# Optimization experiments

Hardware: AMD Instinct MI355X
Metric: run time of the kernel (lower is better)

Reference implementation:

```python
import jax, jax.numpy as jnp
import numpy as np

NUM_USERS = 100000
NUM_ITEMS = 200000
D = 128          # embedding_dim
K = 4            # num interest heads
B = 4096
H = 256          # history length
H1, H2 = 512, 256  # hidden_units


def setup_inputs() -> dict:
    key = jax.random.key(0)
    ks = jax.random.split(key, 10)
    inp = {
        "user_ids": jax.random.randint(ks[0], (B,), 0, NUM_USERS),
        "candidate_items": jax.random.randint(ks[1], (B,), 0, NUM_ITEMS),
        "history_items": jax.random.randint(ks[2], (B, H), 0, NUM_ITEMS),
        "item_table": jax.random.normal(ks[3], (NUM_ITEMS, D), dtype=jnp.float32) * 0.05,
        "Wp": jax.random.normal(ks[4], (D, K), dtype=jnp.float32) * (1.0 / np.sqrt(D)),
        "W1": jax.random.normal(ks[5], (2 * D, H1), dtype=jnp.float32) * (1.0 / np.sqrt(2 * D)),
        "b1": jnp.zeros((H1,), dtype=jnp.float32),
        "W2": jax.random.normal(ks[6], (H1, H2), dtype=jnp.float32) * (1.0 / np.sqrt(H1)),
        "b2": jnp.zeros((H2,), dtype=jnp.float32),
        "W3": jax.random.normal(ks[7], (H2, 1), dtype=jnp.float32) * (1.0 / np.sqrt(H2)),
        "b3": jnp.zeros((1,), dtype=jnp.float32),
    }
    return inp


def reference(user_ids, candidate_items, history_items, item_table, Wp,
              W1, b1, W2, b2, W3, b3):
    # user_ids is unused by the original forward (user_emb never applied)
    item_vecs = item_table[history_items]          # (B, H, D)
    cand_vec = item_table[candidate_items]         # (B, D)

    # per-interest attention scores, softmax over history axis
    scores = jnp.einsum('bhd,dk->bhk', item_vecs, Wp)   # (B, H, K)
    scores = jax.nn.softmax(scores, axis=1)

    # softmax-weighted pooling -> K interest vectors per user
    interest_vectors = jnp.einsum('bhk,bhd->bkd', scores, item_vecs)  # (B, K, D)

    # similarity to candidate, pick best interest (data-dependent gather)
    sim_scores = jnp.einsum('bkd,bd->bk', interest_vectors, cand_vec)  # (B, K)
    best_idx = jnp.argmax(sim_scores, axis=-1)                          # (B,)
    selected = jnp.take_along_axis(
        interest_vectors, best_idx[:, None, None], axis=1)[:, 0, :]    # (B, D)

    # MLP tail: [2D -> 512] ReLU [512 -> 256] ReLU [256 -> 1], sigmoid
    x = jnp.concatenate([selected, cand_vec], axis=-1)  # (B, 2D)
    x = jax.nn.relu(x @ W1 + b1)
    x = jax.nn.relu(x @ W2 + b2)
    out = (x @ W3 + b3)[:, 0]                            # (B,)
    return jax.nn.sigmoid(out)
```

## Files before the change

### kernel.cpp

```cpp
#include <hip/hip_runtime.h>
#include <hip/hip_bf16.h>
#include <math.h>

#define B_SZ   4096
#define H_LEN  256
#define D_DIM  128
#define K_HEADS 4
#define H1_DIM 512
#define H2_DIM 256

#define CH     64
#define NCH    4
#define TPAD   132

typedef __attribute__((ext_vector_type(8))) short bf16x8;
typedef __attribute__((ext_vector_type(4))) float f32x4;

__global__ __launch_bounds__(256, 4) void interest_kernel(
    const int*   __restrict__ cand_ids,
    const int*   __restrict__ hist,
    const float* __restrict__ table,
    const float* __restrict__ Wp,
    __hip_bfloat16* __restrict__ Xbf)
{
    __shared__ float tile[CH * TPAD];
    __shared__ float wpt[K_HEADS * D_DIM];
    __shared__ float exps4[CH * 4];
    __shared__ float candv[D_DIM];
    __shared__ int   rowids[H_LEN];
    __shared__ float lsumW[16];
    __shared__ float simred[4][K_HEADS];
    __shared__ int   bestk;

    const int b    = blockIdx.x;
    const int t    = threadIdx.x;
    const int lane = t & 63, w = t >> 6;
    const int r    = t >> 2, q = t & 3;
    const int d    = t & 127, half = t >> 7;

    if (t < D_DIM) {
        float4 w4 = ((const float4*)Wp)[t];
        wpt[0 * D_DIM + t] = w4.x;
        wpt[1 * D_DIM + t] = w4.y;
        wpt[2 * D_DIM + t] = w4.z;
        wpt[3 * D_DIM + t] = w4.w;
    }
    const int cand = cand_ids[b];
    if (t >= 128 && t < 160) {
        int c = t - 128;
        ((float4*)candv)[c] = ((const float4*)(table + (long long)cand * D_DIM))[c];
    }
    rowids[t] = hist[(long long)b * H_LEN + t];

    __syncthreads();

    float a0 = 0.f, a1 = 0.f, a2 = 0.f, a3 = 0.f;
    float l0 = 0.f, l1 = 0.f, l2 = 0.f, l3 = 0.f;

    float4 v0, v1, v2, v3, v4, v5, v6, v7;
    {
        const int row = rowids[r];
        const float* rp = table + (long long)row * D_DIM + (q << 2);
        v0 = *(const float4*)(rp + 0 * 16);
        v1 = *(const float4*)(rp + 1 * 16);
        v2 = *(const float4*)(rp + 2 * 16);
        v3 = *(const float4*)(rp + 3 * 16);
        v4 = *(const float4*)(rp + 4 * 16);
        v5 = *(const float4*)(rp + 5 * 16);
        v6 = *(const float4*)(rp + 6 * 16);
        v7 = *(const float4*)(rp + 7 * 16);
    }

    #pragma unroll
    for (int c = 0; c < NCH; ++c) {
        float4 u0, u1, u2, u3, u4, u5, u6, u7;
        if (c + 1 < NCH) {
            const int row = rowids[((c + 1) << 6) + r];
            const float* rp = table + (long long)row * D_DIM + (q << 2);
            u0 = *(const float4*)(rp + 0 * 16);
            u1 = *(const float4*)(rp + 1 * 16);
            u2 = *(const float4*)(rp + 2 * 16);
            u3 = *(const float4*)(rp + 3 * 16);
            u4 = *(const float4*)(rp + 4 * 16);
            u5 = *(const float4*)(rp + 5 * 16);
            u6 = *(const float4*)(rp + 6 * 16);
            u7 = *(const float4*)(rp + 7 * 16);
        }

        float s0 = 0.f, s1 = 0.f, s2 = 0.f, s3 = 0.f;
        float4 va;
        #define DO_J(J, VV)                                                     \
        {   va = VV;                                                            \
            const int cb = (q << 2) + (J << 4);                                 \
            float4 w0 = *(const float4*)(wpt + 0 * D_DIM + cb);                 \
            float4 w1 = *(const float4*)(wpt + 1 * D_DIM + cb);                 \
            float4 w2 = *(const float4*)(wpt + 2 * D_DIM + cb);                 \
            float4 w3 = *(const float4*)(wpt + 3 * D_DIM + cb);                 \
            s0 += va.x * w0.x + va.y * w0.y + va.z * w0.z + va.w * w0.w;        \
            s1 += va.x * w1.x + va.y * w1.y + va.z * w1.z + va.w * w1.w;        \
            s2 += va.x * w2.x + va.y * w2.y + va.z * w2.z + va.w * w2.w;        \
            s3 += va.x * w3.x + va.y * w3.y + va.z * w3.z + va.w * w3.w;        \
            *(float4*)(tile + (t >> 2) * TPAD + cb) = va;                       \
        }
        DO_J(0, v0) DO_J(1, v1) DO_J(2, v2) DO_J(3, v3)
        DO_J(4, v4) DO_J(5, v5) DO_J(6, v6) DO_J(7, v7)
        #undef DO_J

        s0 += __shfl_xor(s0, 1); s0 += __shfl_xor(s0, 2);
        s1 += __shfl_xor(s1, 1); s1 += __shfl_xor(s1, 2);
        s2 += __shfl_xor(s2, 1); s2 += __shfl_xor(s2, 2);
        s3 += __shfl_xor(s3, 1); s3 += __shfl_xor(s3, 2);

        float e0 = expf(s0), e1 = expf(s1), e2 = expf(s2), e3 = expf(s3);
        if (q == 0) ((float4*)exps4)[r] = make_float4(e0, e1, e2, e3);

        float t0 = e0, t1 = e1, t2 = e2, t3 = e3;
        #pragma unroll
        for (int off = 4; off <= 32; off <<= 1) {
            t0 += __shfl_xor(t0, off);
            t1 += __shfl_xor(t1, off);
            t2 += __shfl_xor(t2, off);
            t3 += __shfl_xor(t3, off);
        }
        l0 += t0; l1 += t1; l2 += t2; l3 += t3;

        __syncthreads();

        #pragma unroll 8
        for (int i = 0; i < 32; ++i) {
            int hl = (half << 5) + i;
            float4 e4 = ((const float4*)exps4)[hl];
            float  vv = tile[hl * TPAD + d];
            a0 += e4.x * vv; a1 += e4.y * vv; a2 += e4.z * vv; a3 += e4.w * vv;
        }

        __syncthreads();

        v0 = u0; v1 = u1; v2 = u2; v3 = u3;
        v4 = u4; v5 = u5; v6 = u6; v7 = u7;
    }

    float* partBp = tile;
    float* ivbufp = tile + 512;

    if (half == 1) ((float4*)partBp)[d] = make_float4(a0, a1, a2, a3);
    if (lane == 0) ((float4*)lsumW)[w]  = make_float4(l0, l1, l2, l3);
    __syncthreads();

    float s0 = 0.f, s1 = 0.f, s2 = 0.f, s3 = 0.f;
    if (half == 0) {
        float4 pb = ((const float4*)partBp)[d];
        float4 L0 = ((const float4*)lsumW)[0];
        float4 L1 = ((const float4*)lsumW)[1];
        float4 L2 = ((const float4*)lsumW)[2];
        float4 L3 = ((const float4*)lsumW)[3];
        float i0 = 1.f / (L0.x + L1.x + L2.x + L3.x);
        float i1 = 1.f / (L0.y + L1.y + L2.y + L3.y);
        float i2 = 1.f / (L0.z + L1.z + L2.z + L3.z);
        float i3 = 1.f / (L0.w + L1.w + L2.w + L3.w);
        a0 = (a0 + pb.x) * i0;
        a1 = (a1 + pb.y) * i1;
        a2 = (a2 + pb.z) * i2;
        a3 = (a3 + pb.w) * i3;
        ((float4*)ivbufp)[d] = make_float4(a0, a1, a2, a3);
        float cd = candv[d];
        s0 = a0 * cd; s1 = a1 * cd; s2 = a2 * cd; s3 = a3 * cd;
    }
    #pragma unroll
    for (int off = 32; off >= 1; off >>= 1) {
        s0 += __shfl_xor(s0, off);
        s1 += __shfl_xor(s1, off);
        s2 += __shfl_xor(s2, off);
        s3 += __shfl_xor(s3, off);
    }
    if (lane == 0) {
        simred[w][0] = s0; simred[w][1] = s1;
        simred[w][2] = s2; simred[w][3] = s3;
    }
    __syncthreads();

    if (t == 0) {
        float sim[4];
        #pragma unroll
        for (int k = 0; k < 4; ++k)
            sim[k] = simred[0][k] + simred[1][k] + simred[2][k] + simred[3][k];
        int best = 0;
        #pragma unroll
        for (int k = 1; k < 4; ++k) if (sim[k] > sim[best]) best = k;
        bestk = best;
    }
    __syncthreads();

    __hip_bfloat16* xrow = Xbf + (long long)b * (2 * D_DIM);
    if (t < 128) xrow[t] = __float2bfloat16(ivbufp[t * 4 + bestk]);
    else         xrow[t] = __float2bfloat16(candv[t - 128]);
}

__global__ __launch_bounds__(256) void convert_weights(
    const float* __restrict__ W1, const float* __restrict__ W2,
    __hip_bfloat16* __restrict__ W1t, __hip_bfloat16* __restrict__ W2t)
{
    __shared__ float tl[32][33];
    int bid = blockIdx.x;
    const float* W; __hip_bfloat16* Wt; int K, N;
    if (bid < 128) { W = W1; Wt = W1t; K = 2 * D_DIM; N = H1_DIM; }
    else           { W = W2; Wt = W2t; K = H1_DIM;    N = H2_DIM; bid -= 128; }
    const int ntn = N >> 5;
    const int k0 = (bid / ntn) << 5, n0 = (bid % ntn) << 5;
    const int tx = threadIdx.x & 31, ty = threadIdx.x >> 5;
    #pragma unroll
    for (int j = 0; j < 4; ++j)
        tl[ty + 8 * j][tx] = W[(long long)(k0 + ty + 8 * j) * N + n0 + tx];
    __syncthreads();
    #pragma unroll
    for (int j = 0; j < 4; ++j)
        Wt[(long long)(n0 + ty + 8 * j) * K + k0 + tx] =
            __float2bfloat16(tl[tx][ty + 8 * j]);
}

__global__ __launch_bounds__(512) void mlp_fused(
    const __hip_bfloat16* __restrict__ X,
    const __hip_bfloat16* __restrict__ W1t,
    const float* __restrict__ b1,
    const __hip_bfloat16* __restrict__ W2t,
    const float* __restrict__ b2,
    const float* __restrict__ W3,
    const float* __restrict__ b3,
    float*       __restrict__ out)
{
    __shared__ __hip_bfloat16 h1[16][H1_DIM + 8];
    __shared__ float          h2[16][H2_DIM + 4];

    const int t    = threadIdx.x;
    const int wave = t >> 6, lane = t & 63;
    const int lm   = lane & 15, quad = lane >> 4;
    const int m0   = blockIdx.x * 16;

    const __hip_bfloat16* Ap = X + (long long)(m0 + lm) * (2 * D_DIM) + quad * 8;
    bf16x8 af[8];
    #pragma unroll
    for (int it = 0; it < 8; ++it) af[it] = *(const bf16x8*)(Ap + it * 32);

    #pragma unroll
    for (int tn = 0; tn < 4; ++tn) {
        const int n0 = (wave * 4 + tn) * 16;
        const __hip_bfloat16* Bp = W1t + (long long)(n0 + lm) * (2 * D_DIM) + quad * 8;
        f32x4 acc = {0.f, 0.f, 0.f, 0.f};
        #pragma unroll
        for (int it = 0; it < 8; ++it) {
            bf16x8 bfr = *(const bf16x8*)(Bp + it * 32);
            acc = __builtin_amdgcn_mfma_f32_16x16x32_bf16(af[it], bfr, acc, 0, 0, 0);
        }
        const float bv = b1[n0 + lm];
        #pragma unroll
        for (int i = 0; i < 4; ++i)
            h1[quad * 4 + i][n0 + lm] = __float2bfloat16(fmaxf(acc[i] + bv, 0.f));
    }
    __syncthreads();

    bf16x8 a2[16];
    #pragma unroll
    for (int it = 0; it < 16; ++it)
        a2[it] = *(const bf16x8*)(&h1[lm][quad * 8 + it * 32]);

    #pragma unroll
    for (int tn = 0; tn < 2; ++tn) {
        const int n0 = (wave * 2 + tn) * 16;
        const __hip_bfloat16* Bp = W2t + (long long)(n0 + lm) * H1_DIM + quad * 8;
        f32x4 acc = {0.f, 0.f, 0.f, 0.f};
        #pragma unroll
        for (int it = 0; it < 16; ++it) {
            bf16x8 bfr = *(const bf16x8*)(Bp + it * 32);
            acc = __builtin_amdgcn_mfma_f32_16x16x32_bf16(a2[it], bfr, acc, 0, 0, 0);
        }
        const float bv = b2[n0 + lm];
        #pragma unroll
        for (int i = 0; i < 4; ++i)
            h2[quad * 4 + i][n0 + lm] = fmaxf(acc[i] + bv, 0.f);
    }
    __syncthreads();

    {
        const int row = t >> 5, c = (t & 31) * 8;
        float s = 0.f;
        #pragma unroll
        for (int j = 0; j < 8; ++j) s += h2[row][c + j] * W3[c + j];
        #pragma unroll
        for (int off = 1; off <= 16; off <<= 1) s += __shfl_xor(s, off);
        if ((lane & 31) == 0)
            out[m0 + row] = 1.f / (1.f + expf(-(s + b3[0])));
    }
}

extern "C" void kernel_launch(void* const* d_in, const int* in_sizes, int n_in,
                              void* d_out, int out_size, void* d_ws, size_t ws_size,
                              hipStream_t stream) {
    const int*   cand  = (const int*)  d_in[1];
    const int*   hist  = (const int*)  d_in[2];
    const float* table = (const float*)d_in[3];
    const float* Wp    = (const float*)d_in[4];
    const float* W1    = (const float*)d_in[5];
    const float* b1    = (const float*)d_in[6];
    const float* W2    = (const float*)d_in[7];
    const float* b2    = (const float*)d_in[8];
    const float* W3    = (const float*)d_in[9];
    const float* b3    = (const float*)d_in[10];
    float* out = (float*)d_out;

    char* p = (char*)d_ws;
    __hip_bfloat16* Xbf = (__hip_bfloat16*)p;  p += (size_t)B_SZ * 2 * D_DIM * 2;
    __hip_bfloat16* W1t = (__hip_bfloat16*)p;  p += (size_t)H1_DIM * 2 * D_DIM * 2;
    __hip_bfloat16* W2t = (__hip_bfloat16*)p;

    convert_weights<<<256, 256, 0, stream>>>(W1, W2, W1t, W2t);
    interest_kernel<<<B_SZ, 256, 0, stream>>>(cand, hist, table, Wp, Xbf);
    mlp_fused<<<B_SZ / 16, 512, 0, stream>>>(Xbf, W1t, b1, W2t, b2, W3, b3, out);
}
```

Before: 259.5 us.

## Shrink history chunk to 32 rows and drop register prefetch for higher occupancy

```diff
diff --git a/kernel.cpp b/kernel.cpp
--- a/kernel.cpp
+++ b/kernel.cpp
@@ -9,14 +9,14 @@
 #define H1_DIM 512
 #define H2_DIM 256
 
-#define CH     64
-#define NCH    4
+#define CH     32
+#define NCH    8
 #define TPAD   132
 
 typedef __attribute__((ext_vector_type(8))) short bf16x8;
 typedef __attribute__((ext_vector_type(4))) float f32x4;
 
-__global__ __launch_bounds__(256, 4) void interest_kernel(
+__global__ __launch_bounds__(256, 7) void interest_kernel(
     const int*   __restrict__ cand_ids,
     const int*   __restrict__ hist,
     const float* __restrict__ table,
@@ -35,7 +35,7 @@
     const int b    = blockIdx.x;
     const int t    = threadIdx.x;
     const int lane = t & 63, w = t >> 6;
-    const int r    = t >> 2, q = t & 3;
+    const int r    = t >> 3, q = t & 7;
     const int d    = t & 127, half = t >> 7;
 
     if (t < D_DIM) {
@@ -57,41 +57,19 @@
     float a0 = 0.f, a1 = 0.f, a2 = 0.f, a3 = 0.f;
     float l0 = 0.f, l1 = 0.f, l2 = 0.f, l3 = 0.f;
 
-    float4 v0, v1, v2, v3, v4, v5, v6, v7;
-    {
-        const int row = rowids[r];
+    for (int c = 0; c < NCH; ++c) {
+        const int   row = rowids[(c << 5) + r];
         const float* rp = table + (long long)row * D_DIM + (q << 2);
-        v0 = *(const float4*)(rp + 0 * 16);
-        v1 = *(const float4*)(rp + 1 * 16);
-        v2 = *(const float4*)(rp + 2 * 16);
-        v3 = *(const float4*)(rp + 3 * 16);
-        v4 = *(const float4*)(rp + 4 * 16);
-        v5 = *(const float4*)(rp + 5 * 16);
-        v6 = *(const float4*)(rp + 6 * 16);
-        v7 = *(const float4*)(rp + 7 * 16);
-    }
-
-    #pragma unroll
-    for (int c = 0; c < NCH; ++c) {
-        float4 u0, u1, u2, u3, u4, u5, u6, u7;
-        if (c + 1 < NCH) {
-            const int row = rowids[((c + 1) << 6) + r];
-            const float* rp = table + (long long)row * D_DIM + (q << 2);
-            u0 = *(const float4*)(rp + 0 * 16);
-            u1 = *(const float4*)(rp + 1 * 16);
-            u2 = *(const float4*)(rp + 2 * 16);
-            u3 = *(const float4*)(rp + 3 * 16);
-            u4 = *(const float4*)(rp + 4 * 16);
-            u5 = *(const float4*)(rp + 5 * 16);
-            u6 = *(const float4*)(rp + 6 * 16);
-            u7 = *(const float4*)(rp + 7 * 16);
-        }
+        float4 v0 = *(const float4*)(rp + 0 * 32);
+        float4 v1 = *(const float4*)(rp + 1 * 32);
+        float4 v2 = *(const float4*)(rp + 2 * 32);
+        float4 v3 = *(const float4*)(rp + 3 * 32);
 
         float s0 = 0.f, s1 = 0.f, s2 = 0.f, s3 = 0.f;
         float4 va;
-        #define DO_J(J, VV)                                                     \
+        #define DO_J(JJ, VV)                                                    \
         {   va = VV;                                                            \
-            const int cb = (q << 2) + (J << 4);                                 \
+            const int cb = (q << 2) + (JJ << 5);                                \
             float4 w0 = *(const float4*)(wpt + 0 * D_DIM + cb);                 \
             float4 w1 = *(const float4*)(wpt + 1 * D_DIM + cb);                 \
             float4 w2 = *(const float4*)(wpt + 2 * D_DIM + cb);                 \
@@ -100,23 +78,22 @@
             s1 += va.x * w1.x + va.y * w1.y + va.z * w1.z + va.w * w1.w;        \
             s2 += va.x * w2.x + va.y * w2.y + va.z * w2.z + va.w * w2.w;        \
             s3 += va.x * w3.x + va.y * w3.y + va.z * w3.z + va.w * w3.w;        \
-            *(float4*)(tile + (t >> 2) * TPAD + cb) = va;                       \
+            *(float4*)(tile + r * TPAD + cb) = va;                              \
         }
         DO_J(0, v0) DO_J(1, v1) DO_J(2, v2) DO_J(3, v3)
-        DO_J(4, v4) DO_J(5, v5) DO_J(6, v6) DO_J(7, v7)
         #undef DO_J
 
-        s0 += __shfl_xor(s0, 1); s0 += __shfl_xor(s0, 2);
-        s1 += __shfl_xor(s1, 1); s1 += __shfl_xor(s1, 2);
-        s2 += __shfl_xor(s2, 1); s2 += __shfl_xor(s2, 2);
-        s3 += __shfl_xor(s3, 1); s3 += __shfl_xor(s3, 2);
+        s0 += __shfl_xor(s0, 1); s0 += __shfl_xor(s0, 2); s0 += __shfl_xor(s0, 4);
+        s1 += __shfl_xor(s1, 1); s1 += __shfl_xor(s1, 2); s1 += __shfl_xor(s1, 4);
+        s2 += __shfl_xor(s2, 1); s2 += __shfl_xor(s2, 2); s2 += __shfl_xor(s2, 4);
+        s3 += __shfl_xor(s3, 1); s3 += __shfl_xor(s3, 2); s3 += __shfl_xor(s3, 4);
 
         float e0 = expf(s0), e1 = expf(s1), e2 = expf(s2), e3 = expf(s3);
         if (q == 0) ((float4*)exps4)[r] = make_float4(e0, e1, e2, e3);
 
         float t0 = e0, t1 = e1, t2 = e2, t3 = e3;
         #pragma unroll
-        for (int off = 4; off <= 32; off <<= 1) {
+        for (int off = 8; off <= 32; off <<= 1) {
             t0 += __shfl_xor(t0, off);
             t1 += __shfl_xor(t1, off);
             t2 += __shfl_xor(t2, off);
@@ -126,18 +103,15 @@
 
         __syncthreads();
 
-        #pragma unroll 8
-        for (int i = 0; i < 32; ++i) {
-            int hl = (half << 5) + i;
+        #pragma unroll
+        for (int i = 0; i < 16; ++i) {
+            int hl = (half << 4) + i;
             float4 e4 = ((const float4*)exps4)[hl];
             float  vv = tile[hl * TPAD + d];
             a0 += e4.x * vv; a1 += e4.y * vv; a2 += e4.z * vv; a3 += e4.w * vv;
         }
 
         __syncthreads();
-
-        v0 = u0; v1 = u1; v2 = u2; v3 = u3;
-        v4 = u4; v5 = u5; v6 = u6; v7 = u7;
     }
 
     float* partBp = tile;
```

Measured after the change: 282.0 us. 8.7% more time.
